# Optimization experiments

Hardware: AMD Instinct MI355X
Metric: run time of the kernel (lower is better)

Reference implementation:

```python
import jax, jax.numpy as jnp
import numpy as np

B, S, D = 2, 2048, 2048
H, KVH, HD = 16, 8, 128          # heads, kv heads, head_dim
KVR = 512                        # kv_lora_rank
THETA, ROPE_FACTOR = 10000.0, 40.0
EPS = 1e-5
NEG = -1e9


def _layernorm(x, scale):
    mean = jnp.mean(x, axis=-1, keepdims=True)
    var = jnp.mean(jnp.square(x - mean), axis=-1, keepdims=True)
    return (x - mean) * jax.lax.rsqrt(var + EPS) * scale


def _rope_cos_sin(position_ids):
    # freqs over half the head dim, scaled by rope_factor (as in source)
    freqs = (1.0 / THETA ** (jnp.arange(0, HD, 2, dtype=jnp.float32) / HD)) * ROPE_FACTOR
    ang = position_ids.astype(jnp.float32)[:, None] * freqs[None, :]  # [S, HD//2]
    return jnp.cos(ang)[None, :, None, :], jnp.sin(ang)[None, :, None, :]


def _apply_rope(x, cos, sin):
    # x: [B,S,h,HD] with interleaved (real, imag) pairs
    x_ = x.reshape(*x.shape[:-1], -1, 2)
    xr, xi = x_[..., 0], x_[..., 1]
    out = jnp.stack([xr * cos - xi * sin, xr * sin + xi * cos], axis=-1)
    return out.reshape(x.shape)


def setup_inputs() -> dict:
    key = jax.random.key(0)
    ks = jax.random.split(key, 6)
    std = 0.02
    x = jax.random.normal(ks[0], (B, S, D), jnp.float32)
    wq = jax.random.normal(ks[1], (D, H * 2 * HD), jnp.float32) * std
    wkv_a = jax.random.normal(ks[2], (D, KVR + HD), jnp.float32) * std
    kv_norm_scale = jnp.ones((KVR,), jnp.float32)
    wkv_b = jax.random.normal(ks[3], (KVR, KVH * 2 * HD), jnp.float32) * std
    wo = jax.random.normal(ks[4], (H * HD, D), jnp.float32) * std
    causal = jnp.tril(jnp.ones((S, S), bool))
    attention_mask = jnp.where(causal, 0.0, NEG)[None, None].astype(jnp.float32)
    position_ids = jnp.arange(S, dtype=jnp.int32)
    return {"x": x, "wq": wq, "wkv_a": wkv_a, "kv_norm_scale": kv_norm_scale,
            "wkv_b": wkv_b, "wo": wo, "attention_mask": attention_mask,
            "position_ids": position_ids}


def reference(x, wq, wkv_a, kv_norm_scale, wkv_b, wo, attention_mask, position_ids):
    cos, sin = _rope_cos_sin(position_ids)
    # Q path: low-rank disabled (q_lora_rank=0) -> single projection
    q = (x @ wq).reshape(B, S, H, 2 * HD)
    q_nope, q_pe = q[..., :HD], q[..., HD:]
    q = jnp.concatenate([q_nope, _apply_rope(q_pe, cos, sin)], axis=-1)  # [B,S,H,2HD]
    # KV path: low-rank compression + decoupled rope key
    kv = x @ wkv_a                               # [B,S,KVR+HD]
    kv_c = _layernorm(kv[..., :KVR], kv_norm_scale)
    k_pe = kv[..., KVR:]                         # [B,S,HD]
    kvb = (kv_c @ wkv_b).reshape(B, S, KVH, 2 * HD)
    k_nope, v = kvb[..., :HD], kvb[..., HD:]
    k_pe = _apply_rope(k_pe[:, :, None, :], cos, sin)  # [B,S,1,HD]
    k = jnp.concatenate([k_nope, jnp.broadcast_to(k_pe, (B, S, KVH, HD))], axis=-1)
    # GQA expansion
    rep = H // KVH
    k = jnp.repeat(k, rep, axis=2)
    v = jnp.repeat(v, rep, axis=2)
    scale = HD ** -0.5
    scores = jnp.einsum('bqhd,bkhd->bhqk', q, k) * scale + attention_mask
    probs = jax.nn.softmax(scores, axis=-1)
    attn = jnp.einsum('bhqk,bkhd->bqhd', probs, v).reshape(B, S, H * HD)
    return attn @ wo
```

## Files before the change

### kernel.cpp

```cpp
#include <hip/hip_runtime.h>


typedef __attribute__((ext_vector_type(8))) short short8;
typedef __attribute__((ext_vector_type(4))) float floatx4;
typedef unsigned short u16;
typedef unsigned int u32;

__device__ __forceinline__ float bf2f(u16 u){ u32 x=((u32)u)<<16; return __builtin_bit_cast(float,x); }
__device__ __forceinline__ u16 f2bf(float f){ u32 x=__builtin_bit_cast(u32,f); return (u16)((x + 0x7fffu + ((x>>16)&1u))>>16); }

__device__ __forceinline__ floatx4 mfma16(short8 a, short8 b, floatx4 c){
  return __builtin_amdgcn_mfma_f32_16x16x32_bf16(a,b,c,0,0,0);
}

__device__ __forceinline__ void gl_lds16(const u16* g, u16* l){
  __builtin_amdgcn_global_load_lds((const __attribute__((address_space(1))) void*)g,
                                   (__attribute__((address_space(3))) void*)l, 16, 0, 0);
}

__global__ __launch_bounds__(256)
void k_f2b(const float* __restrict__ in, u16* __restrict__ out, size_t n){
  size_t i = ((size_t)blockIdx.x*256 + threadIdx.x)*4;
  if(i >= n) return;
  float4 v = *(const float4*)(in + i);
  out[i+0] = f2bf(v.x); out[i+1] = f2bf(v.y); out[i+2] = f2bf(v.z); out[i+3] = f2bf(v.w);
}

__global__ void k_transpose(const float* __restrict__ in, u16* __restrict__ out, int K, int N){
  __shared__ u16 tile[32][33];
  const int kb = blockIdx.y*32, nb = blockIdx.x*32;
  const int tx = threadIdx.x, ty = threadIdx.y;
#pragma unroll
  for(int i=0;i<4;i++) tile[ty+i*8][tx] = f2bf(in[(size_t)(kb+ty+i*8)*N + nb + tx]);
  __syncthreads();
#pragma unroll
  for(int i=0;i<4;i++) out[(size_t)(nb+ty+i*8)*K + kb + tx] = tile[tx][ty+i*8];
}

__global__ void k_rope_table(float* __restrict__ cosT, float* __restrict__ sinT){
  int idx = blockIdx.x*256 + threadIdx.x;
  if(idx >= 2048*64) return;
  int p = idx>>6, i = idx&63;
  double freq = pow(10000.0, -(double)(2*i)/128.0) * 40.0;
  float ff = (float)freq;
  float ang = (float)((double)p * (double)ff);
  cosT[idx] = (float)cos((double)ang);
  sinT[idx] = (float)sin((double)ang);
}

template<int OUTF32>
__global__ __launch_bounds__(256)
void k_gemm_bt(const u16* __restrict__ A, const u16* __restrict__ Bt, void* __restrict__ Cout,
               int M, int N, int K){
  __shared__ __align__(16) u16 ls[2][2][8192];
  const int t = threadIdx.x;
  const int nbx = N>>7;
  const int nwg = gridDim.x;
  const int swz = (blockIdx.x & 7)*(nwg>>3) + (blockIdx.x>>3);
  const int by = swz / nbx, bx = swz - by*nbx;
  const int m0 = by*128, n0 = bx*128;
  const int wv = t>>6, ln = t&63;
  const int wr = (wv>>1)*64, wc = (wv&1)*64;
  const int fr = ln&15, gq = ln>>4;
  const int srow = t>>3;
  const int suX = (t&7) ^ (srow&7);
  const u16* Ag = A + (size_t)(m0 + srow)*K + suX*8;
  const u16* Bg = Bt + (size_t)(n0 + srow)*K + suX*8;
  const int nt = K>>6;
  const int uk0 = ((gq)     ^ (fr&7))*8;
  const int uk1 = ((4|gq)   ^ (fr&7))*8;
  int raw[4], rbw[4];
#pragma unroll
  for(int i=0;i<4;i++){ raw[i] = (wr+i*16+fr)*64; rbw[i] = (wc+i*16+fr)*64; }

  floatx4 acc[4][4];
#pragma unroll
  for(int i=0;i<4;i++)
#pragma unroll
    for(int j=0;j<4;j++) acc[i][j] = (floatx4){0.f,0.f,0.f,0.f};

  auto stage = [&](int buf, int kt){
    const int k0 = kt*64;
#pragma unroll
    for(int j=0;j<4;j++) gl_lds16(Ag + (size_t)(j*32)*K + k0, &ls[buf][0][j*2048 + t*8]);
#pragma unroll
    for(int j=0;j<4;j++) gl_lds16(Bg + (size_t)(j*32)*K + k0, &ls[buf][1][j*2048 + t*8]);
  };

  stage(0, 0);
  stage(1, 1);
  asm volatile("s_waitcnt vmcnt(8)" ::: "memory");
  __builtin_amdgcn_sched_barrier(0);
  __builtin_amdgcn_s_barrier();
  __builtin_amdgcn_sched_barrier(0);

  for(int kt=0; kt<nt; kt++){
    const int buf = kt&1;
    const u16* LA = &ls[buf][0][0];
    const u16* LB = &ls[buf][1][0];
    __builtin_amdgcn_s_setprio(1);
#pragma unroll
    for(int ks=0; ks<2; ks++){
      const int uk = ks ? uk1 : uk0;
      short8 af[4], bf[4];
#pragma unroll
      for(int i=0;i<4;i++) af[i] = *(const short8*)&LA[raw[i] + uk];
#pragma unroll
      for(int i=0;i<4;i++) bf[i] = *(const short8*)&LB[rbw[i] + uk];
#pragma unroll
      for(int mi=0;mi<4;mi++)
#pragma unroll
        for(int ni=0;ni<4;ni++) acc[mi][ni] = mfma16(af[mi], bf[ni], acc[mi][ni]);
    }
    __builtin_amdgcn_s_setprio(0);
    if(kt+1 < nt){
      asm volatile("s_waitcnt lgkmcnt(0)" ::: "memory");
      __builtin_amdgcn_sched_barrier(0);
      __builtin_amdgcn_s_barrier();
      __builtin_amdgcn_sched_barrier(0);
      if(kt+2 < nt){
        stage(buf, kt+2);
        asm volatile("s_waitcnt vmcnt(8)" ::: "memory");
      } else {
        asm volatile("s_waitcnt vmcnt(0)" ::: "memory");
      }
      __builtin_amdgcn_sched_barrier(0);
      __builtin_amdgcn_s_barrier();
      __builtin_amdgcn_sched_barrier(0);
    }
  }

  const int r0 = gq*4, c0 = fr;
#pragma unroll
  for(int mi=0;mi<4;mi++)
#pragma unroll
    for(int ni=0;ni<4;ni++){
      const int row = m0 + wr + mi*16 + r0;
      const int col = n0 + wc + ni*16 + c0;
#pragma unroll
      for(int r=0;r<4;r++){
        float v = acc[mi][ni][r];
        if(OUTF32) ((float*)Cout)[(size_t)(row+r)*N + col] = v;
        else       ((u16*)Cout)[(size_t)(row+r)*N + col] = f2bf(v);
      }
    }
}

__global__ __launch_bounds__(256)
void k_ln_rope(const float* __restrict__ kv, const float* __restrict__ scale,
               const int* __restrict__ pid, const float* __restrict__ cosT,
               const float* __restrict__ sinT, u16* __restrict__ kv_cn, u16* __restrict__ k_pe){
  const int tok = blockIdx.x;
  const int t = threadIdx.x;
  const float* row = kv + (size_t)tok*640;
  float v0 = row[2*t], v1 = row[2*t+1];
  float s = v0+v1, ss = v0*v0+v1*v1;
#pragma unroll
  for(int off=32; off>=1; off>>=1){ s += __shfl_xor(s,off); ss += __shfl_xor(ss,off); }
  __shared__ float red[8];
  if((t&63)==0){ red[t>>6]=s; red[4+(t>>6)]=ss; }
  __syncthreads();
  float S4 = red[0]+red[1]+red[2]+red[3];
  float SS4 = red[4]+red[5]+red[6]+red[7];
  float mean = S4*(1.f/512.f);
  float var = SS4*(1.f/512.f) - mean*mean;
  float inv = rsqrtf(var + 1e-5f);
  kv_cn[(size_t)tok*512 + 2*t]   = f2bf((v0-mean)*inv*scale[2*t]);
  kv_cn[(size_t)tok*512 + 2*t+1] = f2bf((v1-mean)*inv*scale[2*t+1]);
  if(t < 128){
    const int sidx = tok & 2047;
    const int p = pid[sidx];
    const int i = t>>1;
    float c = cosT[p*64+i], sn = sinT[p*64+i];
    float xr = row[512+2*i], xi = row[512+2*i+1];
    float val = (t&1) ? (xr*sn + xi*c) : (xr*c - xi*sn);
    k_pe[(size_t)tok*128 + t] = f2bf(val);
  }
}

__global__ __launch_bounds__(256)
void k_q_rope(const u16* __restrict__ q_raw, const int* __restrict__ pid,
              const float* __restrict__ cosT, const float* __restrict__ sinT,
              u16* __restrict__ q_fin){
  const float QS = (float)(0.08838834764831845 * 1.4426950408889634);
  const int tok = blockIdx.x;
  const int b = tok>>11, sidx = tok&2047;
  const int t = threadIdx.x;
  const int p = pid[sidx];
  const int h = t>>4, seg = t&15;
  const u16* src = q_raw + (size_t)tok*4096 + h*256 + seg*16;
  u16* dst = q_fin + (((size_t)(b*16 + h))*2048 + sidx)*256 + seg*16;
  short8 a = *(const short8*)src;
  short8 bv = *(const short8*)(src+8);
  short8 oa, ob;
  if(seg < 8){
#pragma unroll
    for(int j=0;j<8;j++){
      oa[j] = (short)f2bf(bf2f((u16)a[j])*QS);
      ob[j] = (short)f2bf(bf2f((u16)bv[j])*QS);
    }
  } else {
    const int i0 = seg*8 - 64;
#pragma unroll
    for(int j=0;j<4;j++){
      float c = cosT[p*64 + i0 + j], sn = sinT[p*64 + i0 + j];
      float xr = bf2f((u16)a[2*j]), xi = bf2f((u16)a[2*j+1]);
      oa[2*j]   = (short)f2bf((xr*c - xi*sn)*QS);
      oa[2*j+1] = (short)f2bf((xr*sn + xi*c)*QS);
    }
#pragma unroll
    for(int j=0;j<4;j++){
      float c = cosT[p*64 + i0 + 4 + j], sn = sinT[p*64 + i0 + 4 + j];
      float xr = bf2f((u16)bv[2*j]), xi = bf2f((u16)bv[2*j+1]);
      ob[2*j]   = (short)f2bf((xr*c - xi*sn)*QS);
      ob[2*j+1] = (short)f2bf((xr*sn + xi*c)*QS);
    }
  }
  *(short8*)dst = oa;
  *(short8*)(dst+8) = ob;
}

__global__ __launch_bounds__(256)
void k_build_k(const u16* __restrict__ kvb, const u16* __restrict__ k_pe, u16* __restrict__ k_full){
  const int tok = blockIdx.x;
  const int b = tok>>11, sidx = tok&2047;
  const int t = threadIdx.x;
  const int kh = t>>5, seg = t&31;
  short8 v;
  if(seg < 16) v = *(const short8*)(kvb + (size_t)tok*2048 + kh*256 + seg*8);
  else         v = *(const short8*)(k_pe + (size_t)tok*128 + (seg-16)*8);
  *(short8*)(k_full + (((size_t)(b*8 + kh))*2048 + sidx)*256 + seg*8) = v;
}

__global__ void k_v_t(const u16* __restrict__ kvb, u16* __restrict__ v_t){
  __shared__ u16 tile[32][33];
  const int sb = blockIdx.x*32, hb = blockIdx.y*32;
  const int bk = blockIdx.z;
  const int b = bk>>3, kh = bk&7;
  const int tx = threadIdx.x, ty = threadIdx.y;
#pragma unroll
  for(int i=0;i<4;i++){
    int sidx = sb + ty + i*8;
    tile[ty+i*8][tx] = kvb[((size_t)(b*2048 + sidx))*2048 + kh*256 + 128 + hb + tx];
  }
  __syncthreads();
#pragma unroll
  for(int i=0;i<4;i++){
    int hd = hb + ty + i*8;
    v_t[(((size_t)bk*64 + blockIdx.x)*128 + hd)*32 + tx] = tile[tx][ty+i*8];
  }
}

__global__ __launch_bounds__(128, 2)
void k_attn(const u16* __restrict__ q_fin, const u16* __restrict__ k_full,
            const u16* __restrict__ v_t, u16* __restrict__ attn){
  __shared__ __align__(16) u16 lsK[2*8192];
  __shared__ __align__(16) u16 lsP[2*32*40];
  const int blk = blockIdx.x;
  const int kvh = blk&7;
  const int i  = blk>>3;
  const int j  = i>>5;
  const int mm = i&31;
  const int s  = mm>>2;
  int qt;
  if(j==0)      qt = s;
  else if(j==1) qt = 31 - s;
  else if(j==2) qt = 8 + s;
  else          qt = 23 - s;
  const int bb = (mm>>1)&1;
  const int hp = mm&1;
  const int h  = kvh*2 + hp;
  const int t = threadIdx.x, wv = t>>6, ln = t&63;
  const int fq = ln&15, gq = ln>>4;
  const u16* kbase = k_full + ((size_t)(bb*8 + kvh))*2048*256;
  const u16* vbase = v_t + ((size_t)(bb*8 + kvh))*128*2048;
  u16* Pw = &lsP[wv*32*40];

  int soff[8];
#pragma unroll
  for(int s8=0;s8<8;s8++){
    int o = s8*2048 + t*16;
    int row = o>>9, colb = o&511;
    soff[s8] = row*512 + (colb ^ ((row&7)<<4));
  }
  const int swz = (fq&7)<<4;
  int cb[8];
#pragma unroll
  for(int c=0;c<8;c++) cb[c] = (gq*16 + c*64) ^ swz;
  const int rowb = fq*512;
  const u16* vfp = vbase + (size_t)fq*32 + gq*8;

  const int last = 2*qt + 1;
  short8 qf[2][8];
#pragma unroll
  for(int m=0;m<2;m++){
    const u16* qb = q_fin + (((size_t)(bb*16 + h))*2048 + qt*64 + wv*32 + m*16 + fq)*256;
#pragma unroll
    for(int c=0;c<8;c++) qf[m][c] = *(const short8*)(qb + c*32 + gq*8);
  }
  floatx4 oacc[2][8];
#pragma unroll
  for(int m=0;m<2;m++)
#pragma unroll
    for(int ii=0;ii<8;ii++) oacc[m][ii] = (floatx4){0.f,0.f,0.f,0.f};
  float mprev0 = -3e38f, mprev1 = -3e38f, lsum0 = 0.f, lsum1 = 0.f;

#pragma unroll
  for(int s8=0;s8<8;s8++)
    gl_lds16((const u16*)((const char*)kbase + soff[s8]), &lsK[s8*1024 + wv*512]);
  __syncthreads();

  int cur = 0;
  for(int kt=0; kt<=last; kt++){
    if(kt < last){
      const char* ktile = (const char*)kbase + (size_t)(kt+1)*16384;
      u16* kdst = &lsK[(cur^1)*8192];
#pragma unroll
      for(int s8=0;s8<8;s8++)
        gl_lds16((const u16*)(ktile + soff[s8]), kdst + s8*1024 + wv*512);
    }
    short8 vf[8];
#pragma unroll
    for(int hs=0;hs<8;hs++)
      vf[hs] = *(const short8*)(vfp + (size_t)kt*4096 + hs*512);

    const char* Kc = (const char*)lsK + cur*16384;
    floatx4 sc[2][2];
#pragma unroll
    for(int m=0;m<2;m++)
#pragma unroll
      for(int ns=0;ns<2;ns++) sc[m][ns] = (floatx4){0.f,0.f,0.f,0.f};
#pragma unroll
    for(int ns=0;ns<2;ns++){
#pragma unroll
      for(int c=0;c<8;c++){
        short8 kf = *(const short8*)(Kc + ns*8192 + rowb + cb[c]);
        sc[0][ns] = mfma16(kf, qf[0][c], sc[0][ns]);
        sc[1][ns] = mfma16(kf, qf[1][c], sc[1][ns]);
      }
    }
    if(kt >= 2*qt){
      const int off = (kt - 2*qt)*32;
#pragma unroll
      for(int m=0;m<2;m++){
        const int qloc = wv*32 + m*16 + fq;
#pragma unroll
        for(int ns=0;ns<2;ns++)
#pragma unroll
          for(int r=0;r<4;r++)
            if(off + ns*16 + gq*4 + r > qloc) sc[m][ns][r] = -1e30f;
      }
    }
    float ml0 = -3e38f, ml1 = -3e38f;
#pragma unroll
    for(int ns=0;ns<2;ns++)
#pragma unroll
      for(int r=0;r<4;r++){ ml0 = fmaxf(ml0, sc[0][ns][r]); ml1 = fmaxf(ml1, sc[1][ns][r]); }
    ml0 = fmaxf(ml0, __shfl_xor(ml0, 16)); ml0 = fmaxf(ml0, __shfl_xor(ml0, 32));
    ml1 = fmaxf(ml1, __shfl_xor(ml1, 16)); ml1 = fmaxf(ml1, __shfl_xor(ml1, 32));
    if(__any((ml0 > mprev0 + 8.f) || (ml1 > mprev1 + 8.f))){
      const float mn0 = fmaxf(mprev0, ml0), mn1 = fmaxf(mprev1, ml1);
      const float a0 = exp2f(mprev0 - mn0), a1 = exp2f(mprev1 - mn1);
      lsum0 *= a0; lsum1 *= a1;
      float aO0[4], aO1[4];
#pragma unroll
      for(int r=0;r<4;r++){ aO0[r] = __shfl(a0, gq*4 + r); aO1[r] = __shfl(a1, gq*4 + r); }
#pragma unroll
      for(int hs=0;hs<8;hs++)
#pragma unroll
        for(int r=0;r<4;r++){ oacc[0][hs][r] *= aO0[r]; oacc[1][hs][r] *= aO1[r]; }
      mprev0 = mn0; mprev1 = mn1;
    }
    float ps0 = 0.f, ps1 = 0.f;
#pragma unroll
    for(int ns=0;ns<2;ns++)
#pragma unroll
      for(int r=0;r<4;r++){
        float p0 = exp2f(sc[0][ns][r] - mprev0);
        float p1 = exp2f(sc[1][ns][r] - mprev1);
        sc[0][ns][r] = p0; sc[1][ns][r] = p1;
        ps0 += p0; ps1 += p1;
      }
    ps0 += __shfl_xor(ps0, 16); ps0 += __shfl_xor(ps0, 32);
    ps1 += __shfl_xor(ps1, 16); ps1 += __shfl_xor(ps1, 32);
    lsum0 += ps0; lsum1 += ps1;

#pragma unroll
    for(int m=0;m<2;m++)
#pragma unroll
      for(int ns=0;ns<2;ns++){
        u32 p01, p23;
        asm("v_cvt_pk_bf16_f32 %0, %1, %2" : "=v"(p01) : "v"(sc[m][ns][0]), "v"(sc[m][ns][1]));
        asm("v_cvt_pk_bf16_f32 %0, %1, %2" : "=v"(p23) : "v"(sc[m][ns][2]), "v"(sc[m][ns][3]));
        uint2 pk; pk.x = p01; pk.y = p23;
        *(uint2*)&Pw[(m*16 + fq)*40 + ns*16 + gq*4] = pk;
      }
    __builtin_amdgcn_s_waitcnt(0xC07F);

#pragma unroll
    for(int m=0;m<2;m++){
      short8 pa = *(const short8*)&Pw[(m*16 + fq)*40 + gq*8];
#pragma unroll
      for(int hs=0;hs<8;hs++)
        oacc[m][hs] = mfma16(pa, vf[hs], oacc[m][hs]);
    }
    __syncthreads();
    cur ^= 1;
  }
  const float i0 = 1.f / lsum0, i1 = 1.f / lsum1;
  float iO0[4], iO1[4];
#pragma unroll
  for(int r=0;r<4;r++){ iO0[r] = __shfl(i0, gq*4 + r); iO1[r] = __shfl(i1, gq*4 + r); }
#pragma unroll
  for(int m=0;m<2;m++)
#pragma unroll
    for(int hs=0;hs<8;hs++)
#pragma unroll
      for(int r=0;r<4;r++){
        const int qi = qt*64 + wv*32 + m*16 + gq*4 + r;
        float sc_ = (m==0) ? iO0[r] : iO1[r];
        attn[(((size_t)(bb*2048 + qi))*16 + h)*128 + hs*16 + fq] = f2bf(oacc[m][hs][r]*sc_);
      }
}

extern "C" void kernel_launch(void* const* d_in, const int* in_sizes, int n_in,
                              void* d_out, int out_size, void* d_ws, size_t ws_size,
                              hipStream_t stream){
  const float* x    = (const float*)d_in[0];
  const float* wq   = (const float*)d_in[1];
  const float* wkva = (const float*)d_in[2];
  const float* kvsc = (const float*)d_in[3];
  const float* wkvb = (const float*)d_in[4];
  const float* wo   = (const float*)d_in[5];
  const int* pid  = (const int*)d_in[7];
  float* out = (float*)d_out;

  char* w = (char*)d_ws;
  size_t off = 0;
  auto alloc = [&](size_t bytes)->void*{
    void* p = (void*)(w + off);
    off += (bytes + 255) & ~(size_t)255;
    return p;
  };
  u16*   x_bf   = (u16*)alloc((size_t)4096*2048*2);
  u16*   wq_t   = (u16*)alloc((size_t)4096*2048*2);
  u16*   wkva_t = (u16*)alloc((size_t)640*2048*2);
  u16*   wkvb_t = (u16*)alloc((size_t)2048*512*2);
  u16*   wo_t   = (u16*)alloc((size_t)2048*2048*2);
  float* cosT   = (float*)alloc((size_t)2048*64*4);
  float* sinT   = (float*)alloc((size_t)2048*64*4);
  u16*   q_raw  = (u16*)alloc((size_t)4096*4096*2);
  float* kvf    = (float*)alloc((size_t)4096*640*4);
  u16*   kv_cn  = (u16*)alloc((size_t)4096*512*2);
  u16*   k_pe   = (u16*)alloc((size_t)4096*128*2);
  u16*   kvb    = (u16*)alloc((size_t)4096*2048*2);
  u16*   q_fin  = (u16*)alloc((size_t)4096*4096*2);
  u16*   k_full = (u16*)alloc((size_t)2*8*2048*256*2);
  u16*   v_t    = (u16*)alloc((size_t)2*8*128*2048*2);
  u16*   attn   = (u16*)alloc((size_t)4096*2048*2);

  k_f2b<<<8192, 256, 0, stream>>>(x, x_bf, (size_t)4096*2048);
  k_transpose<<<dim3(128, 64), dim3(32,8), 0, stream>>>(wq,   wq_t,   2048, 4096);
  k_transpose<<<dim3(20,  64), dim3(32,8), 0, stream>>>(wkva, wkva_t, 2048, 640);
  k_transpose<<<dim3(64,  16), dim3(32,8), 0, stream>>>(wkvb, wkvb_t, 512,  2048);
  k_transpose<<<dim3(64,  64), dim3(32,8), 0, stream>>>(wo,   wo_t,   2048, 2048);
  k_rope_table<<<512, 256, 0, stream>>>(cosT, sinT);

  k_gemm_bt<0><<<1024, 256, 0, stream>>>(x_bf, wq_t, q_raw, 4096, 4096, 2048);
  k_gemm_bt<1><<<160,  256, 0, stream>>>(x_bf, wkva_t, kvf, 4096, 640, 2048);
  k_ln_rope<<<4096, 256, 0, stream>>>(kvf, kvsc, pid, cosT, sinT, kv_cn, k_pe);
  k_gemm_bt<0><<<512,  256, 0, stream>>>(kv_cn, wkvb_t, kvb, 4096, 2048, 512);
  k_q_rope<<<4096, 256, 0, stream>>>(q_raw, pid, cosT, sinT, q_fin);
  k_build_k<<<4096, 256, 0, stream>>>(kvb, k_pe, k_full);
  k_v_t<<<dim3(64, 4, 16), dim3(32,8), 0, stream>>>(kvb, v_t);
  k_attn<<<1024, 128, 0, stream>>>(q_fin, k_full, v_t, attn);
  k_gemm_bt<1><<<512,  256, 0, stream>>>(attn, wo_t, out, 4096, 2048, 2048);
}
```

Before: 466.1 us.

## Pre-swizzle K into MFMA fragment layout and use single-wave attention blocks

The K builder now writes keys in the exact per-lane MFMA fragment order, so the attention kernel loads K fragments straight from global memory into registers. This removes the LDS double-buffer, the async global-to-LDS copies and the per-iteration block barrier. The attention kernel drops to one 64-thread wave per block covering a 32-row query tile, with 2048 blocks and a simpler causal mask on the diagonal tile only. The cost is that two waves sharing a KV head no longer share K loads through LDS, so global and L2 K traffic doubles, and each load is exposed latency with no explicit prefetch.

Result: slower. 526.8 us (+13.0%).

```diff
diff --git a/kernel.cpp b/kernel.cpp
--- a/kernel.cpp
+++ b/kernel.cpp
@@ -221,15 +221,18 @@
 }
 
 __global__ __launch_bounds__(256)
-void k_build_k(const u16* __restrict__ kvb, const u16* __restrict__ k_pe, u16* __restrict__ k_full){
+void k_kfrag(const u16* __restrict__ kvb, const u16* __restrict__ k_pe, u16* __restrict__ k_frag){
   const int tok = blockIdx.x;
-  const int b = tok>>11, sidx = tok&2047;
+  const int bb = tok>>11, sidx = tok&2047;
+  const int kt = sidx>>5, w = sidx&31, ns = w>>4, fq = w&15;
   const int t = threadIdx.x;
-  const int kh = t>>5, seg = t&31;
+  const int kvh = t>>5, c = (t>>2)&7, j = t&3;
+  const int d0 = c*32 + j*8;
   short8 v;
-  if(seg < 16) v = *(const short8*)(kvb + (size_t)tok*2048 + kh*256 + seg*8);
-  else         v = *(const short8*)(k_pe + (size_t)tok*128 + (seg-16)*8);
-  *(short8*)(k_full + (((size_t)(b*8 + kh))*2048 + sidx)*256 + seg*8) = v;
+  if(d0 < 128) v = *(const short8*)(kvb + (size_t)tok*2048 + kvh*256 + d0);
+  else         v = *(const short8*)(k_pe + (size_t)tok*128 + (d0-128));
+  const int g = bb*8 + kvh;
+  *(short8*)(k_frag + (((size_t)g*64 + kt)*16 + ns*8 + c)*512 + fq*32 + j*8) = v;
 }
 
 __global__ void k_v_t(const u16* __restrict__ kvb, u16* __restrict__ v_t){
@@ -251,50 +254,30 @@
   }
 }
 
-__global__ __launch_bounds__(128, 2)
-void k_attn(const u16* __restrict__ q_fin, const u16* __restrict__ k_full,
+__global__ __launch_bounds__(64, 2)
+void k_attn(const u16* __restrict__ q_fin, const u16* __restrict__ k_frag,
             const u16* __restrict__ v_t, u16* __restrict__ attn){
-  __shared__ __align__(16) u16 lsK[2*8192];
-  __shared__ __align__(16) u16 lsP[2*32*40];
-  const int blk = blockIdx.x;
-  const int kvh = blk&7;
-  const int i  = blk>>3;
-  const int j  = i>>5;
-  const int mm = i&31;
-  const int s  = mm>>2;
-  int qt;
-  if(j==0)      qt = s;
-  else if(j==1) qt = 31 - s;
-  else if(j==2) qt = 8 + s;
-  else          qt = 23 - s;
-  const int bb = (mm>>1)&1;
-  const int hp = mm&1;
-  const int h  = kvh*2 + hp;
-  const int t = threadIdx.x, wv = t>>6, ln = t&63;
+  __shared__ __align__(16) u16 lsP[32*40];
+  const int d = blockIdx.x;
+  const int kvh = d&7;
+  const int bb  = (d>>3)&1;
+  const int s   = (d>>4)&7;
+  const int hp  = (d>>7)&1;
+  const int k8  = d>>8;
+  const int kk  = k8>>1;
+  const int u   = (k8&1) ? (63 - kk*8 - s) : (kk*8 + s);
+  const int h   = kvh*2 + hp;
+  const int ln = threadIdx.x & 63;
   const int fq = ln&15, gq = ln>>4;
-  const u16* kbase = k_full + ((size_t)(bb*8 + kvh))*2048*256;
-  const u16* vbase = v_t + ((size_t)(bb*8 + kvh))*128*2048;
-  u16* Pw = &lsP[wv*32*40];
-
-  int soff[8];
-#pragma unroll
-  for(int s8=0;s8<8;s8++){
-    int o = s8*2048 + t*16;
-    int row = o>>9, colb = o&511;
-    soff[s8] = row*512 + (colb ^ ((row&7)<<4));
-  }
-  const int swz = (fq&7)<<4;
-  int cb[8];
-#pragma unroll
-  for(int c=0;c<8;c++) cb[c] = (gq*16 + c*64) ^ swz;
-  const int rowb = fq*512;
-  const u16* vfp = vbase + (size_t)fq*32 + gq*8;
-
-  const int last = 2*qt + 1;
+  const int g = bb*8 + kvh;
+  const int po = fq*32 + gq*8;
+  const u16* kfb = k_frag + (size_t)g*524288 + po;
+  const u16* vfp = v_t    + (size_t)g*262144 + po;
+
   short8 qf[2][8];
 #pragma unroll
   for(int m=0;m<2;m++){
-    const u16* qb = q_fin + (((size_t)(bb*16 + h))*2048 + qt*64 + wv*32 + m*16 + fq)*256;
+    const u16* qb = q_fin + (((size_t)(bb*16 + h))*2048 + u*32 + m*16 + fq)*256;
 #pragma unroll
     for(int c=0;c<8;c++) qf[m][c] = *(const short8*)(qb + c*32 + gq*8);
   }
@@ -305,26 +288,12 @@
     for(int ii=0;ii<8;ii++) oacc[m][ii] = (floatx4){0.f,0.f,0.f,0.f};
   float mprev0 = -3e38f, mprev1 = -3e38f, lsum0 = 0.f, lsum1 = 0.f;
 
-#pragma unroll
-  for(int s8=0;s8<8;s8++)
-    gl_lds16((const u16*)((const char*)kbase + soff[s8]), &lsK[s8*1024 + wv*512]);
-  __syncthreads();
-
-  int cur = 0;
-  for(int kt=0; kt<=last; kt++){
-    if(kt < last){
-      const char* ktile = (const char*)kbase + (size_t)(kt+1)*16384;
-      u16* kdst = &lsK[(cur^1)*8192];
-#pragma unroll
-      for(int s8=0;s8<8;s8++)
-        gl_lds16((const u16*)(ktile + soff[s8]), kdst + s8*1024 + wv*512);
-    }
+  for(int kt=0; kt<=u; kt++){
     short8 vf[8];
 #pragma unroll
     for(int hs=0;hs<8;hs++)
       vf[hs] = *(const short8*)(vfp + (size_t)kt*4096 + hs*512);
 
-    const char* Kc = (const char*)lsK + cur*16384;
     floatx4 sc[2][2];
 #pragma unroll
     for(int m=0;m<2;m++)
@@ -332,23 +301,25 @@
       for(int ns=0;ns<2;ns++) sc[m][ns] = (floatx4){0.f,0.f,0.f,0.f};
 #pragma unroll
     for(int ns=0;ns<2;ns++){
+      short8 kf[8];
+#pragma unroll
+      for(int c=0;c<8;c++)
+        kf[c] = *(const short8*)(kfb + (size_t)kt*8192 + (ns*8+c)*512);
 #pragma unroll
       for(int c=0;c<8;c++){
-        short8 kf = *(const short8*)(Kc + ns*8192 + rowb + cb[c]);
-        sc[0][ns] = mfma16(kf, qf[0][c], sc[0][ns]);
-        sc[1][ns] = mfma16(kf, qf[1][c], sc[1][ns]);
-      }
-    }
-    if(kt >= 2*qt){
-      const int off = (kt - 2*qt)*32;
+        sc[0][ns] = mfma16(kf[c], qf[0][c], sc[0][ns]);
+        sc[1][ns] = mfma16(kf[c], qf[1][c], sc[1][ns]);
+      }
+    }
+    if(kt == u){
 #pragma unroll
       for(int m=0;m<2;m++){
-        const int qloc = wv*32 + m*16 + fq;
+        const int qloc = m*16 + fq;
 #pragma unroll
         for(int ns=0;ns<2;ns++)
 #pragma unroll
           for(int r=0;r<4;r++)
-            if(off + ns*16 + gq*4 + r > qloc) sc[m][ns][r] = -1e30f;
+            if(ns*16 + gq*4 + r > qloc) sc[m][ns][r] = -1e30f;
       }
     }
     float ml0 = -3e38f, ml1 = -3e38f;
@@ -393,19 +364,17 @@
         asm("v_cvt_pk_bf16_f32 %0, %1, %2" : "=v"(p01) : "v"(sc[m][ns][0]), "v"(sc[m][ns][1]));
         asm("v_cvt_pk_bf16_f32 %0, %1, %2" : "=v"(p23) : "v"(sc[m][ns][2]), "v"(sc[m][ns][3]));
         uint2 pk; pk.x = p01; pk.y = p23;
-        *(uint2*)&Pw[(m*16 + fq)*40 + ns*16 + gq*4] = pk;
+        *(uint2*)&lsP[(m*16 + fq)*40 + ns*16 + gq*4] = pk;
       }
     __builtin_amdgcn_s_waitcnt(0xC07F);
 
 #pragma unroll
     for(int m=0;m<2;m++){
-      short8 pa = *(const short8*)&Pw[(m*16 + fq)*40 + gq*8];
+      short8 pa = *(const short8*)&lsP[(m*16 + fq)*40 + gq*8];
 #pragma unroll
       for(int hs=0;hs<8;hs++)
         oacc[m][hs] = mfma16(pa, vf[hs], oacc[m][hs]);
     }
-    __syncthreads();
-    cur ^= 1;
   }
   const float i0 = 1.f / lsum0, i1 = 1.f / lsum1;
   float iO0[4], iO1[4];
@@ -417,7 +386,7 @@
     for(int hs=0;hs<8;hs++)
 #pragma unroll
       for(int r=0;r<4;r++){
-        const int qi = qt*64 + wv*32 + m*16 + gq*4 + r;
+        const int qi = u*32 + m*16 + gq*4 + r;
         float sc_ = (m==0) ? iO0[r] : iO1[r];
         attn[(((size_t)(bb*2048 + qi))*16 + h)*128 + hs*16 + fq] = f2bf(oacc[m][hs][r]*sc_);
       }
@@ -455,7 +424,7 @@
   u16*   k_pe   = (u16*)alloc((size_t)4096*128*2);
   u16*   kvb    = (u16*)alloc((size_t)4096*2048*2);
   u16*   q_fin  = (u16*)alloc((size_t)4096*4096*2);
-  u16*   k_full = (u16*)alloc((size_t)2*8*2048*256*2);
+  u16*   k_frag = (u16*)alloc((size_t)2*8*2048*256*2);
   u16*   v_t    = (u16*)alloc((size_t)2*8*128*2048*2);
   u16*   attn   = (u16*)alloc((size_t)4096*2048*2);
 
@@ -471,8 +440,8 @@
   k_ln_rope<<<4096, 256, 0, stream>>>(kvf, kvsc, pid, cosT, sinT, kv_cn, k_pe);
   k_gemm_bt<0><<<512,  256, 0, stream>>>(kv_cn, wkvb_t, kvb, 4096, 2048, 512);
   k_q_rope<<<4096, 256, 0, stream>>>(q_raw, pid, cosT, sinT, q_fin);
-  k_build_k<<<4096, 256, 0, stream>>>(kvb, k_pe, k_full);
+  k_kfrag<<<4096, 256, 0, stream>>>(kvb, k_pe, k_frag);
   k_v_t<<<dim3(64, 4, 16), dim3(32,8), 0, stream>>>(kvb, v_t);
-  k_attn<<<1024, 128, 0, stream>>>(q_fin, k_full, v_t, attn);
+  k_attn<<<2048, 64, 0, stream>>>(q_fin, k_frag, v_t, attn);
   k_gemm_bt<1><<<512,  256, 0, stream>>>(attn, wo_t, out, 4096, 2048, 2048);
 }
```

## Share K/V tiles across both GQA heads in one 256-thread attention block

Applied to the files above, without the earlier changes.

The attention kernel now launches 512 blocks of 4 waves, where each block handles both query heads of one KV head. Two waves take each head. The K tile is loaded into LDS once per block and read by all four waves, which halves K traffic per query and splits the cooperative load across more threads. The block-to-tile schedule changes to pair the short and long causal tiles, replacing the previous interleaved ordering. This costs fewer blocks and possibly lower occupancy, since the launch bounds now give only 256 threads with no minimum-blocks hint, and the larger P buffer uses more shared memory.

After: 555.1 us. 19.1% more time.

```diff
diff --git a/kernel.cpp b/kernel.cpp
--- a/kernel.cpp
+++ b/kernel.cpp
@@ -251,37 +251,32 @@
   }
 }
 
-__global__ __launch_bounds__(128, 2)
+__global__ __launch_bounds__(256)
 void k_attn(const u16* __restrict__ q_fin, const u16* __restrict__ k_full,
             const u16* __restrict__ v_t, u16* __restrict__ attn){
   __shared__ __align__(16) u16 lsK[2*8192];
-  __shared__ __align__(16) u16 lsP[2*32*40];
+  __shared__ __align__(16) u16 lsP[4*32*40];
   const int blk = blockIdx.x;
-  const int kvh = blk&7;
-  const int i  = blk>>3;
-  const int j  = i>>5;
-  const int mm = i&31;
-  const int s  = mm>>2;
-  int qt;
-  if(j==0)      qt = s;
-  else if(j==1) qt = 31 - s;
-  else if(j==2) qt = 8 + s;
-  else          qt = 23 - s;
-  const int bb = (mm>>1)&1;
-  const int hp = mm&1;
+  const int parity = blk&1;
+  const int rest = blk>>1;
+  const int pr  = rest&15;
+  const int bb  = (rest>>4)&1;
+  const int kvh = rest>>5;
+  const int qt  = parity ? (31-pr) : pr;
+  const int t = threadIdx.x, wv = t>>6, ln = t&63;
+  const int hp = wv&1, sh = wv>>1;
   const int h  = kvh*2 + hp;
-  const int t = threadIdx.x, wv = t>>6, ln = t&63;
   const int fq = ln&15, gq = ln>>4;
   const u16* kbase = k_full + ((size_t)(bb*8 + kvh))*2048*256;
   const u16* vbase = v_t + ((size_t)(bb*8 + kvh))*128*2048;
   u16* Pw = &lsP[wv*32*40];
 
-  int soff[8];
-#pragma unroll
-  for(int s8=0;s8<8;s8++){
-    int o = s8*2048 + t*16;
+  int soff[4];
+#pragma unroll
+  for(int s4=0;s4<4;s4++){
+    int o = s4*4096 + wv*1024 + ln*16;
     int row = o>>9, colb = o&511;
-    soff[s8] = row*512 + (colb ^ ((row&7)<<4));
+    soff[s4] = row*512 + (colb ^ ((row&7)<<4));
   }
   const int swz = (fq&7)<<4;
   int cb[8];
@@ -294,7 +289,7 @@
   short8 qf[2][8];
 #pragma unroll
   for(int m=0;m<2;m++){
-    const u16* qb = q_fin + (((size_t)(bb*16 + h))*2048 + qt*64 + wv*32 + m*16 + fq)*256;
+    const u16* qb = q_fin + (((size_t)(bb*16 + h))*2048 + qt*64 + sh*32 + m*16 + fq)*256;
 #pragma unroll
     for(int c=0;c<8;c++) qf[m][c] = *(const short8*)(qb + c*32 + gq*8);
   }
@@ -306,8 +301,8 @@
   float mprev0 = -3e38f, mprev1 = -3e38f, lsum0 = 0.f, lsum1 = 0.f;
 
 #pragma unroll
-  for(int s8=0;s8<8;s8++)
-    gl_lds16((const u16*)((const char*)kbase + soff[s8]), &lsK[s8*1024 + wv*512]);
+  for(int s4=0;s4<4;s4++)
+    gl_lds16((const u16*)((const char*)kbase + soff[s4]), &lsK[s4*2048 + wv*512]);
   __syncthreads();
 
   int cur = 0;
@@ -316,8 +311,8 @@
       const char* ktile = (const char*)kbase + (size_t)(kt+1)*16384;
       u16* kdst = &lsK[(cur^1)*8192];
 #pragma unroll
-      for(int s8=0;s8<8;s8++)
-        gl_lds16((const u16*)(ktile + soff[s8]), kdst + s8*1024 + wv*512);
+      for(int s4=0;s4<4;s4++)
+        gl_lds16((const u16*)(ktile + soff[s4]), kdst + s4*2048 + wv*512);
     }
     short8 vf[8];
 #pragma unroll
@@ -343,7 +338,7 @@
       const int off = (kt - 2*qt)*32;
 #pragma unroll
       for(int m=0;m<2;m++){
-        const int qloc = wv*32 + m*16 + fq;
+        const int qloc = sh*32 + m*16 + fq;
 #pragma unroll
         for(int ns=0;ns<2;ns++)
 #pragma unroll
@@ -417,7 +412,7 @@
     for(int hs=0;hs<8;hs++)
 #pragma unroll
       for(int r=0;r<4;r++){
-        const int qi = qt*64 + wv*32 + m*16 + gq*4 + r;
+        const int qi = qt*64 + sh*32 + m*16 + gq*4 + r;
         float sc_ = (m==0) ? iO0[r] : iO1[r];
         attn[(((size_t)(bb*2048 + qi))*16 + h)*128 + hs*16 + fq] = f2bf(oacc[m][hs][r]*sc_);
       }
@@ -473,6 +468,6 @@
   k_q_rope<<<4096, 256, 0, stream>>>(q_raw, pid, cosT, sinT, q_fin);
   k_build_k<<<4096, 256, 0, stream>>>(kvb, k_pe, k_full);
   k_v_t<<<dim3(64, 4, 16), dim3(32,8), 0, stream>>>(kvb, v_t);
-  k_attn<<<1024, 128, 0, stream>>>(q_fin, k_full, v_t, attn);
+  k_attn<<<512, 256, 0, stream>>>(q_fin, k_full, v_t, attn);
   k_gemm_bt<1><<<512,  256, 0, stream>>>(attn, wo_t, out, 4096, 2048, 2048);
 }
```

## Fuse Q rope/scale and K/V layout scatter into GEMM epilogues

Applied to the files above, without the earlier changes.

The Q projection GEMM epilogue now applies RoPE (using a lane shuffle to get the pair partner) and the softmax scale, then writes directly into the head-major q_fin layout, which removes the q_raw buffer and the separate q_rope pass. The kv_b GEMM epilogue scatters k_nope straight into k_full and writes V directly in the transposed tiled layout, replacing the build_k and v_t kernels. A small kernel fills the shared rope key part of k_full. This cuts intermediate HBM round-trips and kernel launches, at the cost of strided, less coalesced epilogue stores and per-element table loads inside the GEMM.

New measurement: 484.9 us. 1.04x slower.

```diff
diff --git a/kernel.cpp b/kernel.cpp
--- a/kernel.cpp
+++ b/kernel.cpp
@@ -48,10 +48,12 @@
   sinT[idx] = (float)sin((double)ang);
 }
 
-template<int OUTF32>
+template<int MODE>
 __global__ __launch_bounds__(256)
 void k_gemm_bt(const u16* __restrict__ A, const u16* __restrict__ Bt, void* __restrict__ Cout,
-               int M, int N, int K){
+               int M, int N, int K,
+               const int* __restrict__ pid, const float* __restrict__ cosT,
+               const float* __restrict__ sinT, u16* __restrict__ out2){
   __shared__ __align__(16) u16 ls[2][2][8192];
   const int t = threadIdx.x;
   const int nbx = N>>7;
@@ -131,19 +133,80 @@
   }
 
   const int r0 = gq*4, c0 = fr;
-#pragma unroll
-  for(int mi=0;mi<4;mi++)
-#pragma unroll
-    for(int ni=0;ni<4;ni++){
-      const int row = m0 + wr + mi*16 + r0;
-      const int col = n0 + wc + ni*16 + c0;
-#pragma unroll
-      for(int r=0;r<4;r++){
-        float v = acc[mi][ni][r];
-        if(OUTF32) ((float*)Cout)[(size_t)(row+r)*N + col] = v;
-        else       ((u16*)Cout)[(size_t)(row+r)*N + col] = f2bf(v);
-      }
-    }
+  if(MODE <= 1){
+#pragma unroll
+    for(int mi=0;mi<4;mi++)
+#pragma unroll
+      for(int ni=0;ni<4;ni++){
+        const int row = m0 + wr + mi*16 + r0;
+        const int col = n0 + wc + ni*16 + c0;
+#pragma unroll
+        for(int r=0;r<4;r++){
+          float v = acc[mi][ni][r];
+          if(MODE==1) ((float*)Cout)[(size_t)(row+r)*N + col] = v;
+          else        ((u16*)Cout)[(size_t)(row+r)*N + col] = f2bf(v);
+        }
+      }
+  } else if(MODE == 2){
+    const float QS = (float)(0.08838834764831845 * 1.4426950408889634);
+    u16* qf = (u16*)Cout;
+    const bool rope = (n0 & 128) != 0;
+#pragma unroll
+    for(int mi=0;mi<4;mi++)
+#pragma unroll
+      for(int ni=0;ni<4;ni++){
+        const int row = m0 + wr + mi*16 + r0;
+        const int col = n0 + wc + ni*16 + c0;
+        const int h = col>>8, d = col&255;
+#pragma unroll
+        for(int r=0;r<4;r++){
+          const int tok = row + r;
+          const int b = tok>>11, sidx = tok&2047;
+          float v = acc[mi][ni][r];
+          float res;
+          if(rope){
+            const int p = pid[sidx];
+            const int i = (d-128)>>1;
+            float c = cosT[p*64+i], sn = sinT[p*64+i];
+            float partner = __shfl_xor(v, 1);
+            if((c0&1)==0) res = v*c - partner*sn;
+            else          res = partner*sn + v*c;
+          } else {
+            res = v;
+          }
+          qf[(((size_t)(b*16 + h))*2048 + sidx)*256 + d] = f2bf(res*QS);
+        }
+      }
+  } else {
+    u16* kfull = (u16*)Cout;
+    const bool isv = (n0 & 128) != 0;
+#pragma unroll
+    for(int mi=0;mi<4;mi++)
+#pragma unroll
+      for(int ni=0;ni<4;ni++){
+        const int row = m0 + wr + mi*16 + r0;
+        const int col = n0 + wc + ni*16 + c0;
+        const int kvh = (col>>8)&7, dd = col&255;
+        if(!isv){
+#pragma unroll
+          for(int r=0;r<4;r++){
+            const int tok = row + r;
+            const int b = tok>>11, sidx = tok&2047;
+            kfull[(((size_t)(b*8 + kvh))*2048 + sidx)*256 + dd] = f2bf(acc[mi][ni][r]);
+          }
+        } else {
+          const int tok = row;
+          const int b = tok>>11, sidx = tok&2047;
+          const int kt = sidx>>5, kv = sidx&31;
+          const int hd = dd - 128;
+          const size_t base = (((size_t)(b*8 + kvh)*64 + kt)*128 + hd)*32 + kv;
+          u32 lo = (u32)f2bf(acc[mi][ni][0]) | ((u32)f2bf(acc[mi][ni][1])<<16);
+          u32 hi = (u32)f2bf(acc[mi][ni][2]) | ((u32)f2bf(acc[mi][ni][3])<<16);
+          uint2 pk; pk.x = lo; pk.y = hi;
+          *(uint2*)&out2[base] = pk;
+        }
+      }
+  }
 }
 
 __global__ __launch_bounds__(256)
@@ -178,77 +241,14 @@
   }
 }
 
-__global__ __launch_bounds__(256)
-void k_q_rope(const u16* __restrict__ q_raw, const int* __restrict__ pid,
-              const float* __restrict__ cosT, const float* __restrict__ sinT,
-              u16* __restrict__ q_fin){
-  const float QS = (float)(0.08838834764831845 * 1.4426950408889634);
+__global__ __launch_bounds__(128)
+void k_pefill(const u16* __restrict__ k_pe, u16* __restrict__ k_full){
   const int tok = blockIdx.x;
   const int b = tok>>11, sidx = tok&2047;
   const int t = threadIdx.x;
-  const int p = pid[sidx];
-  const int h = t>>4, seg = t&15;
-  const u16* src = q_raw + (size_t)tok*4096 + h*256 + seg*16;
-  u16* dst = q_fin + (((size_t)(b*16 + h))*2048 + sidx)*256 + seg*16;
-  short8 a = *(const short8*)src;
-  short8 bv = *(const short8*)(src+8);
-  short8 oa, ob;
-  if(seg < 8){
-#pragma unroll
-    for(int j=0;j<8;j++){
-      oa[j] = (short)f2bf(bf2f((u16)a[j])*QS);
-      ob[j] = (short)f2bf(bf2f((u16)bv[j])*QS);
-    }
-  } else {
-    const int i0 = seg*8 - 64;
-#pragma unroll
-    for(int j=0;j<4;j++){
-      float c = cosT[p*64 + i0 + j], sn = sinT[p*64 + i0 + j];
-      float xr = bf2f((u16)a[2*j]), xi = bf2f((u16)a[2*j+1]);
-      oa[2*j]   = (short)f2bf((xr*c - xi*sn)*QS);
-      oa[2*j+1] = (short)f2bf((xr*sn + xi*c)*QS);
-    }
-#pragma unroll
-    for(int j=0;j<4;j++){
-      float c = cosT[p*64 + i0 + 4 + j], sn = sinT[p*64 + i0 + 4 + j];
-      float xr = bf2f((u16)bv[2*j]), xi = bf2f((u16)bv[2*j+1]);
-      ob[2*j]   = (short)f2bf((xr*c - xi*sn)*QS);
-      ob[2*j+1] = (short)f2bf((xr*sn + xi*c)*QS);
-    }
-  }
-  *(short8*)dst = oa;
-  *(short8*)(dst+8) = ob;
-}
-
-__global__ __launch_bounds__(256)
-void k_build_k(const u16* __restrict__ kvb, const u16* __restrict__ k_pe, u16* __restrict__ k_full){
-  const int tok = blockIdx.x;
-  const int b = tok>>11, sidx = tok&2047;
-  const int t = threadIdx.x;
-  const int kh = t>>5, seg = t&31;
-  short8 v;
-  if(seg < 16) v = *(const short8*)(kvb + (size_t)tok*2048 + kh*256 + seg*8);
-  else         v = *(const short8*)(k_pe + (size_t)tok*128 + (seg-16)*8);
-  *(short8*)(k_full + (((size_t)(b*8 + kh))*2048 + sidx)*256 + seg*8) = v;
-}
-
-__global__ void k_v_t(const u16* __restrict__ kvb, u16* __restrict__ v_t){
-  __shared__ u16 tile[32][33];
-  const int sb = blockIdx.x*32, hb = blockIdx.y*32;
-  const int bk = blockIdx.z;
-  const int b = bk>>3, kh = bk&7;
-  const int tx = threadIdx.x, ty = threadIdx.y;
-#pragma unroll
-  for(int i=0;i<4;i++){
-    int sidx = sb + ty + i*8;
-    tile[ty+i*8][tx] = kvb[((size_t)(b*2048 + sidx))*2048 + kh*256 + 128 + hb + tx];
-  }
-  __syncthreads();
-#pragma unroll
-  for(int i=0;i<4;i++){
-    int hd = hb + ty + i*8;
-    v_t[(((size_t)bk*64 + blockIdx.x)*128 + hd)*32 + tx] = tile[tx][ty+i*8];
-  }
+  const int kh = t>>4, seg = t&15;
+  short8 v = *(const short8*)(k_pe + (size_t)tok*128 + seg*8);
+  *(short8*)(k_full + (((size_t)(b*8 + kh))*2048 + sidx)*256 + 128 + seg*8) = v;
 }
 
 __global__ __launch_bounds__(128, 2)
@@ -449,11 +449,9 @@
   u16*   wo_t   = (u16*)alloc((size_t)2048*2048*2);
   float* cosT   = (float*)alloc((size_t)2048*64*4);
   float* sinT   = (float*)alloc((size_t)2048*64*4);
-  u16*   q_raw  = (u16*)alloc((size_t)4096*4096*2);
   float* kvf    = (float*)alloc((size_t)4096*640*4);
   u16*   kv_cn  = (u16*)alloc((size_t)4096*512*2);
   u16*   k_pe   = (u16*)alloc((size_t)4096*128*2);
-  u16*   kvb    = (u16*)alloc((size_t)4096*2048*2);
   u16*   q_fin  = (u16*)alloc((size_t)4096*4096*2);
   u16*   k_full = (u16*)alloc((size_t)2*8*2048*256*2);
   u16*   v_t    = (u16*)alloc((size_t)2*8*128*2048*2);
@@ -466,13 +464,15 @@
   k_transpose<<<dim3(64,  64), dim3(32,8), 0, stream>>>(wo,   wo_t,   2048, 2048);
   k_rope_table<<<512, 256, 0, stream>>>(cosT, sinT);
 
-  k_gemm_bt<0><<<1024, 256, 0, stream>>>(x_bf, wq_t, q_raw, 4096, 4096, 2048);
-  k_gemm_bt<1><<<160,  256, 0, stream>>>(x_bf, wkva_t, kvf, 4096, 640, 2048);
+  k_gemm_bt<2><<<1024, 256, 0, stream>>>(x_bf, wq_t, q_fin, 4096, 4096, 2048,
+                                         pid, cosT, sinT, nullptr);
+  k_gemm_bt<1><<<160,  256, 0, stream>>>(x_bf, wkva_t, kvf, 4096, 640, 2048,
+                                         nullptr, nullptr, nullptr, nullptr);
   k_ln_rope<<<4096, 256, 0, stream>>>(kvf, kvsc, pid, cosT, sinT, kv_cn, k_pe);
-  k_gemm_bt<0><<<512,  256, 0, stream>>>(kv_cn, wkvb_t, kvb, 4096, 2048, 512);
-  k_q_rope<<<4096, 256, 0, stream>>>(q_raw, pid, cosT, sinT, q_fin);
-  k_build_k<<<4096, 256, 0, stream>>>(kvb, k_pe, k_full);
-  k_v_t<<<dim3(64, 4, 16), dim3(32,8), 0, stream>>>(kvb, v_t);
+  k_gemm_bt<3><<<512,  256, 0, stream>>>(kv_cn, wkvb_t, k_full, 4096, 2048, 512,
+                                         nullptr, nullptr, nullptr, v_t);
+  k_pefill<<<4096, 128, 0, stream>>>(k_pe, k_full);
   k_attn<<<1024, 128, 0, stream>>>(q_fin, k_full, v_t, attn);
-  k_gemm_bt<1><<<512,  256, 0, stream>>>(attn, wo_t, out, 4096, 2048, 2048);
-}
+  k_gemm_bt<1><<<512,  256, 0, stream>>>(attn, wo_t, out, 4096, 2048, 2048,
+                                         nullptr, nullptr, nullptr, nullptr);
+}
```
